# Performance work log

Measured on AMD Instinct MI355X. Metric: run time of the kernel, lower is better.

Reference implementation:

```python
import jax, jax.numpy as jnp
import numpy as np

N_ATOM, N_QUERY, KNN = 100000, 20000, 32
E = N_QUERY * KNN
HID, EDGE_F, HEADS = 128, 16, 8
D_HEAD = HID // HEADS
LN_EPS = 1e-5


def setup_inputs() -> dict:
    key = jax.random.key(0)
    ks = jax.random.split(key, 16)
    s = 1.0 / np.sqrt(HID)
    src = jax.random.randint(ks[0], (E,), 0, N_ATOM)
    dst = jnp.repeat(jnp.arange(N_QUERY), KNN)  # each query has KNN incoming edges
    return {
        "h_atom": jax.random.normal(ks[1], (N_ATOM, HID), jnp.float32),
        "h_query": jax.random.normal(ks[2], (N_QUERY, HID), jnp.float32),
        "edge_attr": jax.random.uniform(ks[3], (E, EDGE_F), jnp.float32),
        "W_q": jax.random.normal(ks[4], (HID, HID), jnp.float32) * s,
        "W_k": jax.random.normal(ks[5], (HID, HID), jnp.float32) * s,
        "W_v": jax.random.normal(ks[6], (HID, HID), jnp.float32) * s,
        "W_rbf": jax.random.normal(ks[7], (HEADS, EDGE_F), jnp.float32) * (1.0 / np.sqrt(EDGE_F)),
        "W1": jax.random.normal(ks[8], (HID, 2 * HID), jnp.float32) * (1.0 / np.sqrt(2 * HID)),
        "b1": jnp.zeros((HID,), jnp.float32),
        "W2": jax.random.normal(ks[9], (HID, HID), jnp.float32) * s,
        "b2": jnp.zeros((HID,), jnp.float32),
        "ln_gamma": jnp.ones((HID,), jnp.float32),
        "ln_beta": jnp.zeros((HID,), jnp.float32),
        "edge_index": jnp.stack([src, dst]),
        "n_query": N_QUERY,
    }


def reference(h_atom, h_query, edge_attr, W_q, W_k, W_v, W_rbf, W1, b1, W2, b2,
              ln_gamma, ln_beta, edge_index, n_query):
    src, dst = edge_index[0], edge_index[1]
    En = src.shape[0]
    # gather + project, per-edge multi-head Q/K/V  [E, H, d]
    Q = (h_query[dst] @ W_q.T).reshape(En, HEADS, D_HEAD)
    K = (h_atom[src] @ W_k.T).reshape(En, HEADS, D_HEAD)
    V = (h_atom[src] @ W_v.T).reshape(En, HEADS, D_HEAD)
    scores = jnp.einsum("ehd,ehd->eh", Q, K) / np.sqrt(D_HEAD) + edge_attr @ W_rbf.T  # [E,H]
    # segment softmax over edges sharing the same dst query, per head
    seg_max = jax.lax.stop_gradient(jax.ops.segment_max(scores, dst, num_segments=n_query))
    ex = jnp.exp(scores - seg_max[dst])
    denom = jax.ops.segment_sum(ex, dst, num_segments=n_query)
    alpha = ex / (denom[dst] + 1e-16)  # [E,H]
    # weighted scatter-add aggregation
    msgs = (alpha[:, :, None] * V).reshape(En, HID)
    agg = jax.ops.segment_sum(msgs, dst, num_segments=n_query)  # [Nq, HID]
    # update MLP + residual + LayerNorm
    z = jnp.concatenate([h_query, agg], axis=-1)
    delta = jax.nn.relu(z @ W1.T + b1) @ W2.T + b2
    y = h_query + delta
    mu = y.mean(-1, keepdims=True)
    var = y.var(-1, keepdims=True)
    return (y - mu) / jnp.sqrt(var + LN_EPS) * ln_gamma + ln_beta
```

## Files before the change

kernel.cpp:

```cpp
#include <hip/hip_runtime.h>
#include <hip/hip_bf16.h>
#include <math.h>

#define N_ATOM   100000
#define N_QUERY  20000
#define KNN      32

typedef __attribute__((ext_vector_type(8))) short  short8;
typedef __attribute__((ext_vector_type(4))) float  floatx4;
typedef __attribute__((ext_vector_type(2))) float  fx2;

static __device__ __forceinline__ unsigned short f2bf_bits(float f) {
  union { __hip_bfloat16 h; unsigned short u; } cv;
  cv.h = __float2bfloat16(f);
  return cv.u;
}
static __device__ __forceinline__ float bflo(unsigned int u) { return __uint_as_float(u << 16); }
static __device__ __forceinline__ float bfhi(unsigned int u) { return __uint_as_float(u & 0xffff0000u); }

__global__ void pack_all_kernel(const float* __restrict__ Wq, const float* __restrict__ Wk,
                                const float* __restrict__ Wv, const float* __restrict__ W1,
                                const float* __restrict__ W2,
                                unsigned short* __restrict__ WKVp, unsigned short* __restrict__ WQp,
                                unsigned short* __restrict__ W1p,  unsigned short* __restrict__ W2p) {
  int tid = blockIdx.x * blockDim.x + threadIdx.x;
  if (tid >= 98304) return;
  const float *Wa, *Wb; int nsplit, Kd, Nd; unsigned short* dst; float scale = 1.0f;
  int t = tid;
  if (t < 32768)      { Wa = Wk; Wb = Wv; nsplit = 128; Kd = 128; Nd = 256; dst = WKVp; }
  else if (t < 49152) { t -= 32768; Wa = Wq; Wb = Wq; nsplit = 128; Kd = 128; Nd = 128; dst = WQp; scale = 0.25f; }
  else if (t < 81920) { t -= 49152; Wa = W1; Wb = W1; nsplit = 128; Kd = 256; Nd = 128; dst = W1p; }
  else                { t -= 81920; Wa = W2; Wb = W2; nsplit = 128; Kd = 128; Nd = 128; dst = W2p; }
  int j    = t & 7;
  int lane = (t >> 3) & 63;
  int t2   = t >> 9;
  int NT   = Nd >> 4;
  int ntile = t2 % NT;
  int ktile = t2 / NT;
  int k = ktile * 32 + (lane >> 4) * 8 + j;
  int n = ntile * 16 + (lane & 15);
  float v = (n < nsplit) ? Wa[(size_t)n * Kd + k] : Wb[(size_t)(n - nsplit) * Kd + k];
  dst[t] = f2bf_bits(v * scale);
}

template<int KD, int NT, int EPI>
__global__ __launch_bounds__(256) void gemm_k(
    const float* __restrict__ A, const unsigned short* __restrict__ Bp, int M,
    unsigned short* __restrict__ outb, unsigned char* __restrict__ outp8) {
  constexpr int ND = NT * 16;
  const int l    = threadIdx.x & 63;
  const int w    = threadIdx.x >> 6;
  const int quad = l >> 4;
  const int col0 = l & 15;
  const int row0 = blockIdx.x * 64 + w * 16;
  int arow = row0 + col0;
  if (arow >= M) arow = M - 1;

  floatx4 acc[NT];
#pragma unroll
  for (int i = 0; i < NT; i++) acc[i] = (floatx4){0.f, 0.f, 0.f, 0.f};

  const float* aptr = A + (size_t)arow * KD + quad * 8;
#pragma unroll
  for (int k0 = 0; k0 < KD; k0 += 32) {
    floatx4 a0 = *(const floatx4*)(aptr + k0);
    floatx4 a1 = *(const floatx4*)(aptr + k0 + 4);
    short8 af;
    af[0] = (short)f2bf_bits(a0[0]); af[1] = (short)f2bf_bits(a0[1]);
    af[2] = (short)f2bf_bits(a0[2]); af[3] = (short)f2bf_bits(a0[3]);
    af[4] = (short)f2bf_bits(a1[0]); af[5] = (short)f2bf_bits(a1[1]);
    af[6] = (short)f2bf_bits(a1[2]); af[7] = (short)f2bf_bits(a1[3]);
    const unsigned short* bbase = Bp + (size_t)(k0 >> 5) * NT * 512 + l * 8;
#pragma unroll
    for (int nt = 0; nt < NT; nt++) {
      short8 bf = *(const short8*)(bbase + nt * 512);
      acc[nt] = __builtin_amdgcn_mfma_f32_16x16x32_bf16(af, bf, acc[nt], 0, 0, 0);
    }
  }

  if (EPI == 0) {
#pragma unroll
    for (int nt = 0; nt < NT; nt++) {
#pragma unroll
      for (int r = 0; r < 4; r++) {
        int row = row0 + quad * 4 + r;
        if (row < M) outb[(size_t)row * ND + nt * 16 + col0] = f2bf_bits(acc[nt][r]);
      }
    }
  } else {
#pragma unroll
    for (int nt = 0; nt < NT; nt++) {
#pragma unroll
      for (int r = 0; r < 4; r++) {
        int row = row0 + quad * 4 + r;
        if (row < M) {
          int c = nt * 16 + col0;
          if (c < 128) {
            int pk = __builtin_amdgcn_cvt_pk_fp8_f32(acc[nt][r], acc[nt][r], 0, false);
            outp8[(size_t)row * 128 + c] = (unsigned char)(pk & 0xff);
          } else {
            outb[(size_t)row * 128 + (c - 128)] = f2bf_bits(acc[nt][r]);
          }
        }
      }
    }
  }
}

__global__ __launch_bounds__(256) void attn_kernel(
    const unsigned short* __restrict__ Qb,
    const unsigned char* __restrict__ Kp8,
    const unsigned short* __restrict__ Vb,
    const float* __restrict__ edge_attr,
    const float* __restrict__ Wrbf,
    const int* __restrict__ src,
    float* __restrict__ Agg) {
  const int l = threadIdx.x & 63;
  const int w = threadIdx.x >> 6;
  const int q = blockIdx.x * 4 + w;
  const int h  = l >> 3;
  const int r8 = l & 7;

  unsigned int qu = ((const unsigned int*)(Qb + (size_t)q * 128))[l];
  float q0 = bflo(qu);
  float q1 = bfhi(qu);
  float2 wr = *(const float2*)(Wrbf + h * 16 + 2 * r8);

  const int e0 = q * KNN;
  int srcj = (l < KNN) ? src[e0 + l] : 0;

  float lsum = 0.f, acc0 = 0.f, acc1 = 0.f;
#pragma unroll 8
  for (int j = 0; j < KNN; j++) {
    int s = __shfl(srcj, j, 64);
    unsigned int ku = *(const unsigned short*)(Kp8 + (size_t)s * 128 + 2 * l);
    unsigned int vu = ((const unsigned int*)(Vb + (size_t)s * 128))[l];
    float2 ea = *(const float2*)(edge_attr + (size_t)(e0 + j) * 16 + 2 * r8);
    fx2 kf = __builtin_amdgcn_cvt_pk_f32_fp8((int)ku, false);
    float part = q0 * kf[0] + q1 * kf[1] + wr.x * ea.x + wr.y * ea.y;
    part += __shfl_xor(part, 1, 64);
    part += __shfl_xor(part, 2, 64);
    part += __shfl_xor(part, 4, 64);
    float p = __expf(part);
    lsum += p;
    acc0 += p * bflo(vu);
    acc1 += p * bfhi(vu);
  }
  float inv = 1.f / (lsum + 1e-16f);
  float2 ag; ag.x = acc0 * inv; ag.y = acc1 * inv;
  *(float2*)(Agg + (size_t)q * 128 + 2 * l) = ag;
}

__global__ __launch_bounds__(256) void mlp_kernel(
    const float* __restrict__ h_query, const float* __restrict__ Agg,
    const unsigned short* __restrict__ W1p, const unsigned short* __restrict__ W2p,
    const float* __restrict__ b1, const float* __restrict__ b2,
    const float* __restrict__ gamma, const float* __restrict__ beta,
    float* __restrict__ out) {
  constexpr int M = N_QUERY;
  constexpr int STRIDE = 136;
  __shared__ unsigned short hid[64 * STRIDE];

  const int l    = threadIdx.x & 63;
  const int w    = threadIdx.x >> 6;
  const int quad = l >> 4;
  const int col0 = l & 15;
  const int row0 = blockIdx.x * 64 + w * 16;
  int arow = row0 + col0;
  if (arow >= M) arow = M - 1;

  floatx4 acc[8];
#pragma unroll
  for (int i = 0; i < 8; i++) acc[i] = (floatx4){0.f, 0.f, 0.f, 0.f};
#pragma unroll
  for (int k0 = 0; k0 < 256; k0 += 32) {
    const float* sp = (k0 < 128) ? (h_query + (size_t)arow * 128 + k0)
                                 : (Agg + (size_t)arow * 128 + (k0 - 128));
    floatx4 a0 = *(const floatx4*)(sp + quad * 8);
    floatx4 a1 = *(const floatx4*)(sp + quad * 8 + 4);
    short8 af;
    af[0] = (short)f2bf_bits(a0[0]); af[1] = (short)f2bf_bits(a0[1]);
    af[2] = (short)f2bf_bits(a0[2]); af[3] = (short)f2bf_bits(a0[3]);
    af[4] = (short)f2bf_bits(a1[0]); af[5] = (short)f2bf_bits(a1[1]);
    af[6] = (short)f2bf_bits(a1[2]); af[7] = (short)f2bf_bits(a1[3]);
    const unsigned short* bbase = W1p + (size_t)(k0 >> 5) * 8 * 512 + l * 8;
#pragma unroll
    for (int nt = 0; nt < 8; nt++) {
      short8 bf = *(const short8*)(bbase + nt * 512);
      acc[nt] = __builtin_amdgcn_mfma_f32_16x16x32_bf16(af, bf, acc[nt], 0, 0, 0);
    }
  }
#pragma unroll
  for (int nt = 0; nt < 8; nt++) {
#pragma unroll
    for (int r = 0; r < 4; r++) {
      int rl = w * 16 + quad * 4 + r;
      float v = acc[nt][r] + b1[nt * 16 + col0];
      hid[rl * STRIDE + nt * 16 + col0] = f2bf_bits(fmaxf(v, 0.f));
    }
  }
  __syncthreads();

  floatx4 acc2[8];
#pragma unroll
  for (int i = 0; i < 8; i++) acc2[i] = (floatx4){0.f, 0.f, 0.f, 0.f};
  const int rloc = w * 16 + col0;
#pragma unroll
  for (int k0 = 0; k0 < 128; k0 += 32) {
    short8 af = *(const short8*)(hid + rloc * STRIDE + k0 + quad * 8);
    const unsigned short* bbase = W2p + (size_t)(k0 >> 5) * 8 * 512 + l * 8;
#pragma unroll
    for (int nt = 0; nt < 8; nt++) {
      short8 bf = *(const short8*)(bbase + nt * 512);
      acc2[nt] = __builtin_amdgcn_mfma_f32_16x16x32_bf16(af, bf, acc2[nt], 0, 0, 0);
    }
  }

#pragma unroll
  for (int r = 0; r < 4; r++) {
    int row = row0 + quad * 4 + r;
    int rr  = row < M ? row : M - 1;
    float v[8];
    float s1 = 0.f, s2 = 0.f;
#pragma unroll
    for (int nt = 0; nt < 8; nt++) {
      int c = nt * 16 + col0;
      v[nt] = acc2[nt][r] + b2[c] + h_query[(size_t)rr * 128 + c];
      s1 += v[nt];
    }
    s1 += __shfl_xor(s1, 1, 64); s1 += __shfl_xor(s1, 2, 64);
    s1 += __shfl_xor(s1, 4, 64); s1 += __shfl_xor(s1, 8, 64);
#pragma unroll
    for (int nt = 0; nt < 8; nt++) s2 += v[nt] * v[nt];
    s2 += __shfl_xor(s2, 1, 64); s2 += __shfl_xor(s2, 2, 64);
    s2 += __shfl_xor(s2, 4, 64); s2 += __shfl_xor(s2, 8, 64);
    float mean = s1 * (1.0f / 128.0f);
    float var  = s2 * (1.0f / 128.0f) - mean * mean;
    float rstd = rsqrtf(var + 1e-5f);
    if (row < M) {
#pragma unroll
      for (int nt = 0; nt < 8; nt++) {
        int c = nt * 16 + col0;
        out[(size_t)row * 128 + c] = (v[nt] - mean) * rstd * gamma[c] + beta[c];
      }
    }
  }
}

extern "C" void kernel_launch(void* const* d_in, const int* in_sizes, int n_in,
                              void* d_out, int out_size, void* d_ws, size_t ws_size,
                              hipStream_t stream) {
  const float* h_atom    = (const float*)d_in[0];
  const float* h_query   = (const float*)d_in[1];
  const float* edge_attr = (const float*)d_in[2];
  const float* W_q  = (const float*)d_in[3];
  const float* W_k  = (const float*)d_in[4];
  const float* W_v  = (const float*)d_in[5];
  const float* Wrbf = (const float*)d_in[6];
  const float* W1   = (const float*)d_in[7];
  const float* b1   = (const float*)d_in[8];
  const float* W2   = (const float*)d_in[9];
  const float* b2   = (const float*)d_in[10];
  const float* ln_g = (const float*)d_in[11];
  const float* ln_b = (const float*)d_in[12];
  const int* edge_index = (const int*)d_in[13];
  float* out = (float*)d_out;

  char* ws = (char*)d_ws;
  unsigned char*  Kp8 = (unsigned char*)(ws);
  unsigned short* Vb  = (unsigned short*)(ws + 12800000);
  unsigned short* Qb  = (unsigned short*)(ws + 38400000);
  float* Agg          = (float*)(ws + 43520000);
  unsigned short* WKVp = (unsigned short*)(ws + 53760000);
  unsigned short* WQp  = WKVp + 32768;
  unsigned short* W1p  = WQp  + 16384;
  unsigned short* W2p  = W1p  + 32768;

  pack_all_kernel<<<(98304 + 255) / 256, 256, 0, stream>>>(
      W_q, W_k, W_v, W1, W2, WKVp, WQp, W1p, W2p);

  gemm_k<128, 16, 3><<<(N_ATOM + 63) / 64, 256, 0, stream>>>(
      h_atom, WKVp, N_ATOM, Vb, Kp8);
  gemm_k<128, 8, 0><<<(N_QUERY + 63) / 64, 256, 0, stream>>>(
      h_query, WQp, N_QUERY, Qb, nullptr);
  attn_kernel<<<N_QUERY / 4, 256, 0, stream>>>(Qb, Kp8, Vb, edge_attr, Wrbf, edge_index, Agg);
  mlp_kernel<<<(N_QUERY + 63) / 64, 256, 0, stream>>>(
      h_query, Agg, W1p, W2p, b1, b2, ln_g, ln_b, out);
}
```

Measured before the change: 243.9 us.

## Stage K/V GEMM epilogue through LDS and split attention edges across half-waves

The fp8-K/bf16-V GEMM epilogue now writes results into shared memory first, then stores them to global memory as coalesced 16-byte vectors instead of scattered byte and short stores. The attention kernel now has each lane handle four head dimensions with wider loads. Each half-wave processes 16 of the 32 neighbours, and the partial softmax sums and accumulators are combined with a cross-half shuffle at the end. This cuts loop iterations and shuffle steps per edge and widens memory transactions. The cost is more LDS use in the GEMM, a block barrier, and extra reduction shuffles.

After: 251.5 us. +3.1%, slower.

```diff
diff --git a/kernel.cpp b/kernel.cpp
--- a/kernel.cpp
+++ b/kernel.cpp
@@ -48,6 +48,8 @@
     const float* __restrict__ A, const unsigned short* __restrict__ Bp, int M,
     unsigned short* __restrict__ outb, unsigned char* __restrict__ outp8) {
   constexpr int ND = NT * 16;
+  constexpr int LDSB = (EPI == 3) ? 24576 : 16;
+  __shared__ char lds[LDSB];
   const int l    = threadIdx.x & 63;
   const int w    = threadIdx.x >> 6;
   const int quad = l >> 4;
@@ -92,17 +94,29 @@
     for (int nt = 0; nt < NT; nt++) {
 #pragma unroll
       for (int r = 0; r < 4; r++) {
-        int row = row0 + quad * 4 + r;
-        if (row < M) {
-          int c = nt * 16 + col0;
-          if (c < 128) {
-            int pk = __builtin_amdgcn_cvt_pk_fp8_f32(acc[nt][r], acc[nt][r], 0, false);
-            outp8[(size_t)row * 128 + c] = (unsigned char)(pk & 0xff);
-          } else {
-            outb[(size_t)row * 128 + (c - 128)] = f2bf_bits(acc[nt][r]);
-          }
+        int rl = w * 16 + quad * 4 + r;
+        int c  = nt * 16 + col0;
+        if (c < 128) {
+          int pk = __builtin_amdgcn_cvt_pk_fp8_f32(acc[nt][r], acc[nt][r], 0, false);
+          lds[rl * 128 + c] = (char)(pk & 0xff);
+        } else {
+          *(unsigned short*)&lds[8192 + rl * 256 + (c - 128) * 2] = f2bf_bits(acc[nt][r]);
         }
       }
+    }
+    __syncthreads();
+    const int row0g = blockIdx.x * 64;
+#pragma unroll
+    for (int it = 0; it < 2; it++) {
+      int off = threadIdx.x * 16 + it * 4096;
+      if (row0g + (off >> 7) < M)
+        *(float4*)(outp8 + (size_t)row0g * 128 + off) = *(const float4*)&lds[off];
+    }
+#pragma unroll
+    for (int it = 0; it < 4; it++) {
+      int off = threadIdx.x * 16 + it * 4096;
+      if (row0g + (off >> 8) < M)
+        *(float4*)((char*)outb + (size_t)row0g * 256 + off) = *(const float4*)&lds[8192 + off];
     }
   }
 }
@@ -115,40 +129,49 @@
     const float* __restrict__ Wrbf,
     const int* __restrict__ src,
     float* __restrict__ Agg) {
-  const int l = threadIdx.x & 63;
-  const int w = threadIdx.x >> 6;
-  const int q = blockIdx.x * 4 + w;
-  const int h  = l >> 3;
-  const int r8 = l & 7;
-
-  unsigned int qu = ((const unsigned int*)(Qb + (size_t)q * 128))[l];
-  float q0 = bflo(qu);
-  float q1 = bfhi(qu);
-  float2 wr = *(const float2*)(Wrbf + h * 16 + 2 * r8);
+  const int l  = threadIdx.x & 63;
+  const int w  = threadIdx.x >> 6;
+  const int q  = blockIdx.x * 4 + w;
+  const int hw = l >> 5;
+  const int m  = l & 31;
+  const int c  = m & 3;
+
+  uint2 qu = *(const uint2*)(Qb + (size_t)q * 128 + 4 * m);
+  float qd0 = bflo(qu.x), qd1 = bfhi(qu.x), qd2 = bflo(qu.y), qd3 = bfhi(qu.y);
+  float4 wr = *(const float4*)(Wrbf + (m >> 2) * 16 + 4 * c);
 
   const int e0 = q * KNN;
   int srcj = (l < KNN) ? src[e0 + l] : 0;
 
-  float lsum = 0.f, acc0 = 0.f, acc1 = 0.f;
-#pragma unroll 8
-  for (int j = 0; j < KNN; j++) {
-    int s = __shfl(srcj, j, 64);
-    unsigned int ku = *(const unsigned short*)(Kp8 + (size_t)s * 128 + 2 * l);
-    unsigned int vu = ((const unsigned int*)(Vb + (size_t)s * 128))[l];
-    float2 ea = *(const float2*)(edge_attr + (size_t)(e0 + j) * 16 + 2 * r8);
-    fx2 kf = __builtin_amdgcn_cvt_pk_f32_fp8((int)ku, false);
-    float part = q0 * kf[0] + q1 * kf[1] + wr.x * ea.x + wr.y * ea.y;
+  float lsum = 0.f, a0 = 0.f, a1 = 0.f, a2 = 0.f, a3 = 0.f;
+#pragma unroll 4
+  for (int t = 0; t < 16; t++) {
+    int e = hw * 16 + t;
+    int s = __shfl(srcj, e, 64);
+    unsigned int ku = *(const unsigned int*)(Kp8 + (size_t)s * 128 + 4 * m);
+    uint2 vu = *(const uint2*)(Vb + (size_t)s * 128 + 4 * m);
+    float4 ea = *(const float4*)(edge_attr + (size_t)(e0 + e) * 16 + 4 * c);
+    fx2 k01 = __builtin_amdgcn_cvt_pk_f32_fp8((int)ku, false);
+    fx2 k23 = __builtin_amdgcn_cvt_pk_f32_fp8((int)ku, true);
+    float part = qd0 * k01[0] + qd1 * k01[1] + qd2 * k23[0] + qd3 * k23[1]
+               + wr.x * ea.x + wr.y * ea.y + wr.z * ea.z + wr.w * ea.w;
     part += __shfl_xor(part, 1, 64);
     part += __shfl_xor(part, 2, 64);
-    part += __shfl_xor(part, 4, 64);
     float p = __expf(part);
     lsum += p;
-    acc0 += p * bflo(vu);
-    acc1 += p * bfhi(vu);
-  }
+    a0 += p * bflo(vu.x); a1 += p * bfhi(vu.x);
+    a2 += p * bflo(vu.y); a3 += p * bfhi(vu.y);
+  }
+  a0 += __shfl_xor(a0, 32, 64);
+  a1 += __shfl_xor(a1, 32, 64);
+  a2 += __shfl_xor(a2, 32, 64);
+  a3 += __shfl_xor(a3, 32, 64);
+  lsum += __shfl_xor(lsum, 32, 64);
   float inv = 1.f / (lsum + 1e-16f);
-  float2 ag; ag.x = acc0 * inv; ag.y = acc1 * inv;
-  *(float2*)(Agg + (size_t)q * 128 + 2 * l) = ag;
+  if (hw == 0) {
+    float4 o; o.x = a0 * inv; o.y = a1 * inv; o.z = a2 * inv; o.w = a3 * inv;
+    *(float4*)(Agg + (size_t)q * 128 + 4 * m) = o;
+  }
 }
 
 __global__ __launch_bounds__(256) void mlp_kernel(
```
